# Kernel tuning notes

Hardware: AMD Instinct MI355X
Metric: run time of the kernel (lower is better)

## Reference

```python
import jax, jax.numpy as jnp
import numpy as np

N = 100_000       # total nodes
E = 1_600_000     # edges (avg degree 16)
IN, H, L = 16, 64, 32
G = 100           # graphs
NPG = N // G      # nodes per graph (equal-sized graphs)


def _glorot(key, fan_in, fan_out):
    s = np.sqrt(6.0 / (fan_in + fan_out)).astype(np.float32)
    return jax.random.uniform(key, (fan_in, fan_out), jnp.float32, -s, s)


def setup_inputs() -> dict:
    key = jax.random.key(0)
    ks = jax.random.split(key, 6)
    x = jax.random.normal(ks[0], (N, IN), jnp.float32)
    edge_index = jax.random.randint(ks[1], (2, E), 0, N, dtype=jnp.int64)
    batch = jnp.repeat(jnp.arange(G, dtype=jnp.int64), NPG)  # sorted graph ids
    kw = jax.random.split(ks[2], 4)
    return dict(
        x=x, edge_index=edge_index, batch=batch, nodes_per_graph=NPG,
        W1=_glorot(kw[0], IN, H), b1=jnp.zeros((H,), jnp.float32),
        W2=_glorot(kw[1], H, L), b2=jnp.zeros((L,), jnp.float32),
        W3=_glorot(kw[2], L, H), b3=jnp.zeros((H,), jnp.float32),
        W4=_glorot(kw[3], H, IN), b4=jnp.zeros((IN,), jnp.float32),
    )


def _gcn(x, W, b, src, dst, norm, n):
    # GCNConv: out[dst] += norm_e * (x @ W)[src], plus bias
    h = x @ W
    msg = h[src] * norm[:, None]
    return jax.ops.segment_sum(msg, dst, num_segments=n) + b


def reference(x, edge_index, batch, nodes_per_graph,
              W1, b1, W2, b2, W3, b3, W4, b4):
    n = x.shape[0]
    loops = jnp.arange(n, dtype=edge_index.dtype)
    src = jnp.concatenate([edge_index[0], loops])  # add self-loops (PyG default)
    dst = jnp.concatenate([edge_index[1], loops])
    deg = jax.ops.segment_sum(jnp.ones_like(dst, jnp.float32), dst, num_segments=n)
    dis = jax.lax.rsqrt(jnp.maximum(deg, 1.0))  # deg >= 1 from self-loops
    norm = dis[src] * dis[dst]                   # symmetric normalization

    # encode
    h = jax.nn.relu(_gcn(x, W1, b1, src, dst, norm, n))
    h = _gcn(h, W2, b2, src, dst, norm, n)
    g = n // nodes_per_graph
    sums = jax.ops.segment_sum(h, batch, num_segments=g)
    cnts = jax.ops.segment_sum(jnp.ones((n, 1), jnp.float32), batch, num_segments=g)
    z = sums / cnts                              # global_mean_pool -> [G, L]

    # decode: repeat_interleave(bincount(batch)) with equal graph sizes
    zr = jnp.repeat(z, nodes_per_graph, axis=0)  # [N, L]
    d = jax.nn.relu(_gcn(zr, W3, b3, src, dst, norm, n))
    return _gcn(d, W4, b4, src, dst, norm, n)    # [N, IN]
```

## Files before the change

### kernel.cpp

```cpp
#include <hip/hip_runtime.h>
#include <hip/hip_bf16.h>


constexpr int BSZ_LOG = 9;
constexpr int BSZ     = 1 << BSZ_LOG;
constexpr int NBMAX   = 256;
constexpr int ECHUNK  = 8192;
constexpr int BCAP    = 12288;
constexpr int ZSPLIT  = 8;

__device__ __forceinline__ int gdiv(int v, int npg, float inv) {
    int g = __float2int_rz((float)v * inv);
    int r = v - g * npg;
    if (r < 0) --g; else if (r >= npg) ++g;
    return g;
}

__global__ __launch_bounds__(256)
void binfill_kernel(const int* __restrict__ src, const int* __restrict__ dst,
                    int* __restrict__ bcnt, int* __restrict__ binned, int E) {
    __shared__ int hist[NBMAX], hexcl[NBMAX], gbase[NBMAX], hpos[NBMAX], tmp[NBMAX];
    __shared__ int sorted[ECHUNK];
    __shared__ unsigned char bsorted[ECHUNK];
    int t = threadIdx.x;
    hist[t] = 0; hpos[t] = 0;
    __syncthreads();
    int e0 = blockIdx.x * ECHUNK;
    int cnt = min(ECHUNK, E - e0);
    for (int i = t; i < cnt; i += 256)
        atomicAdd(&hist[dst[e0 + i] >> BSZ_LOG], 1);
    __syncthreads();
    tmp[t] = hist[t];
    __syncthreads();
    for (int d = 1; d < 256; d <<= 1) {
        int v = (t >= d) ? tmp[t - d] : 0;
        __syncthreads();
        tmp[t] += v;
        __syncthreads();
    }
    hexcl[t] = (t == 0) ? 0 : tmp[t - 1];
    int h = hist[t];
    gbase[t] = (h > 0) ? atomicAdd(&bcnt[t], h) : 0;
    __syncthreads();
    for (int i = t; i < cnt; i += 256) {
        int s = src[e0 + i], d = dst[e0 + i];
        int b = d >> BSZ_LOG;
        int code = ((d & (BSZ - 1)) << 20) | s;
        int sp = hexcl[b] + atomicAdd(&hpos[b], 1);
        sorted[sp] = code;
        bsorted[sp] = (unsigned char)b;
    }
    __syncthreads();
    for (int i = t; i < cnt; i += 256) {
        int b = bsorted[i];
        binned[(size_t)b * BCAP + gbase[b] + (i - hexcl[b])] = sorted[i];
    }
}

__device__ __forceinline__ int prefix_before(const int* __restrict__ bcnt,
                                             int b, int* sums) {
    int t = threadIdx.x;
    sums[t] = (t < b) ? bcnt[t] : 0;
    __syncthreads();
    for (int d = 128; d > 0; d >>= 1) {
        if (t < d) sums[t] += sums[t + d];
        __syncthreads();
    }
    int r = sums[0];
    __syncthreads();
    return r;
}

__global__ __launch_bounds__(256)
void csr_off_kernel(const int* __restrict__ binned, const int* __restrict__ bcnt,
                    int* __restrict__ off, float* __restrict__ dis, int n, int E) {
    __shared__ int hist[BSZ];
    __shared__ int lstart[BSZ];
    __shared__ int partial[256];
    int b = blockIdx.x, t = threadIdx.x;
    int nb0 = b << BSZ_LOG;
    int nn = min(BSZ, n - nb0);
    int m = bcnt[b];
    int bs = prefix_before(bcnt, b, partial);
    const int* bp = binned + (size_t)b * BCAP;
    for (int i = t; i < BSZ; i += 256) hist[i] = 0;
    __syncthreads();
    for (int i = t; i < m; i += 256)
        atomicAdd(&hist[bp[i] >> 20], 1);
    __syncthreads();
    int a0 = hist[2 * t], a1 = hist[2 * t + 1];
    partial[t] = a0 + a1;
    __syncthreads();
    for (int d = 1; d < 256; d <<= 1) {
        int v = (t >= d) ? partial[t - d] : 0;
        __syncthreads();
        partial[t] += v;
        __syncthreads();
    }
    int base = (t == 0) ? 0 : partial[t - 1];
    lstart[2 * t] = base;
    lstart[2 * t + 1] = base + a0;
    __syncthreads();
    for (int i = t; i < nn; i += 256) {
        off[nb0 + i] = bs + lstart[i];
        dis[nb0 + i] = rsqrtf((float)hist[i] + 1.0f);
    }
    if (b == 0 && t == 0) off[n] = E;
}

__global__ __launch_bounds__(256)
void bucket_scatter_kernel(const int* __restrict__ binned, const int* __restrict__ bcnt,
                           const float* __restrict__ dis,
                           const int* __restrict__ npg_p, int2* __restrict__ ew, int n) {
    __shared__ int lstart[BSZ];
    __shared__ int lpos[BSZ];
    __shared__ float ldis[BSZ];
    __shared__ int partial[256];
    int b = blockIdx.x, t = threadIdx.x;
    int nb0 = b << BSZ_LOG;
    int nn = min(BSZ, n - nb0);
    int m = bcnt[b];
    int e0 = prefix_before(bcnt, b, partial);
    int npg = npg_p[0];
    float inv = 1.0f / (float)npg;
    const int* bp = binned + (size_t)b * BCAP;
    for (int i = t; i < BSZ; i += 256) {
        lstart[i] = 0; lpos[i] = 0;
        ldis[i] = (i < nn) ? dis[nb0 + i] : 0.f;
    }
    __syncthreads();
    for (int i = t; i < m; i += 256)
        atomicAdd(&lstart[bp[i] >> 20], 1);
    __syncthreads();
    int a0 = lstart[2 * t], a1 = lstart[2 * t + 1];
    partial[t] = a0 + a1;
    __syncthreads();
    for (int d = 1; d < 256; d <<= 1) {
        int v = (t >= d) ? partial[t - d] : 0;
        __syncthreads();
        partial[t] += v;
        __syncthreads();
    }
    int base = (t == 0) ? 0 : partial[t - 1];
    lstart[2 * t] = base;
    lstart[2 * t + 1] = base + a0;
    __syncthreads();
    for (int i = t; i < m; i += 256) {
        int code = bp[i];
        int dl = code >> 20, s = code & 0xFFFFF;
        float w = dis[s] * ldis[dl];
        int g = gdiv(s, npg, inv);
        int p = e0 + lstart[dl] + atomicAdd(&lpos[dl], 1);
        ew[p] = make_int2(s | (g << 20), __float_as_int(w));
    }
}

template <int TPN, bool USE_G>
__device__ __forceinline__ float4
edge_loop(const float4* __restrict__ hp, const int2* __restrict__ ew,
          int e0, int e1, int q, float4 acc) {
    int deg = e1 - e0;
    int nfull = deg / TPN;
    int r = deg - nfull * TPN;
    int idx = e0 + q;
    int2 a = make_int2(0, 0);
    if (idx < e1) a = ew[idx];
    for (int c = 0; c < nfull; ++c) {
        int nidx = idx + (c + 1) * TPN;
        int2 an = make_int2(0, 0);
        if (nidx < e1) an = ew[nidx];
#pragma unroll
        for (int k = 0; k < TPN; ++k) {
            int ax = __shfl(a.x, k, TPN);
            float w = __int_as_float(__shfl(a.y, k, TPN));
            int row = USE_G ? (int)(((unsigned)ax) >> 20) : (ax & 0xFFFFF);
            float4 v = hp[(size_t)row * TPN + q];
            acc.x += w * v.x; acc.y += w * v.y; acc.z += w * v.z; acc.w += w * v.w;
        }
        a = an;
    }
    for (int k = 0; k < r; ++k) {
        int ax = __shfl(a.x, k, TPN);
        float w = __int_as_float(__shfl(a.y, k, TPN));
        int row = USE_G ? (int)(((unsigned)ax) >> 20) : (ax & 0xFFFFF);
        float4 v = hp[(size_t)row * TPN + q];
        acc.x += w * v.x; acc.y += w * v.y; acc.z += w * v.z; acc.w += w * v.w;
    }
    return acc;
}

__global__ __launch_bounds__(256)
void l1w2_kernel(const float* __restrict__ x, const float* __restrict__ dis,
                 const int* __restrict__ off, const int2* __restrict__ ew,
                 const float* __restrict__ W1, const float* __restrict__ b1,
                 const float* __restrict__ W2, float* __restrict__ t2, int n) {
    __shared__ float accs[64][17];
    __shared__ float hl[64][65];
    __shared__ float Wl[16 * 64];
    __shared__ float bl[64];
    int t = threadIdx.x;
    for (int i = t; i < 16 * 64; i += 256) Wl[i] = W1[i];
    if (t < 64) bl[t] = b1[t];

    int q = t & 3, ln = t >> 2;
    int node = blockIdx.x * 64 + ln;
    const float4* xp = (const float4*)x;
    float4 acc = make_float4(0.f, 0.f, 0.f, 0.f);
    if (node < n) {
        float di = dis[node], d2 = di * di;
        float4 v = xp[(size_t)node * 4 + q];
        acc.x = d2 * v.x; acc.y = d2 * v.y; acc.z = d2 * v.z; acc.w = d2 * v.w;
        acc = edge_loop<4, false>(xp, ew, off[node], off[node + 1], q, acc);
    }
    accs[ln][q * 4 + 0] = acc.x; accs[ln][q * 4 + 1] = acc.y;
    accs[ln][q * 4 + 2] = acc.z; accs[ln][q * 4 + 3] = acc.w;
    __syncthreads();

    int j = t & 63;
    for (int nb = (t >> 6); nb < 64; nb += 4) {
        float s = bl[j];
#pragma unroll
        for (int k = 0; k < 16; ++k) s += accs[nb][k] * Wl[k * 64 + j];
        hl[nb][j] = fmaxf(s, 0.f);
    }
    __syncthreads();

    int base = blockIdx.x * 64;
    int c = t & 31;
    for (int nb = (t >> 5); nb < 64; nb += 8) {
        int nd = base + nb;
        if (nd >= n) break;
        float s = 0.f;
#pragma unroll
        for (int k = 0; k < 64; ++k) s += hl[nb][k] * W2[k * 32 + c];
        t2[(size_t)nd * 32 + c] = s;
    }
}

template <int WD>
__global__ __launch_bounds__(256)
void agg_kernel(const float* __restrict__ h, const float* __restrict__ dis,
                const int* __restrict__ off, const int2* __restrict__ ew,
                const float* __restrict__ b, float* __restrict__ out, int n) {
    constexpr int TPN = WD / 4;
    constexpr int NPB = 256 / TPN;
    int t = threadIdx.x;
    int q = t % TPN, ln = t / TPN;
    int node = blockIdx.x * NPB + ln;
    if (node >= n) return;
    const float4* hp = (const float4*)h;
    float di = dis[node], d2 = di * di;
    float4 v = hp[(size_t)node * TPN + q];
    float4 acc;
    acc.x = d2 * v.x; acc.y = d2 * v.y; acc.z = d2 * v.z; acc.w = d2 * v.w;
    acc = edge_loop<TPN, false>(hp, ew, off[node], off[node + 1], q, acc);
    float4 bb = ((const float4*)b)[q];
    float4 o;
    o.x = acc.x + bb.x; o.y = acc.y + bb.y; o.z = acc.z + bb.z; o.w = acc.w + bb.w;
    ((float4*)out)[(size_t)node * TPN + q] = o;
}

__global__ __launch_bounds__(256)
void zagg_kernel(const float* __restrict__ t2, const float* __restrict__ dis,
                 const int* __restrict__ off, const int2* __restrict__ ew,
                 const int* __restrict__ npg_p, float* __restrict__ zsum, int n) {
    __shared__ float4 red0[256];
    __shared__ float4 red1[256];
    int blk = blockIdx.x;
    int b = blk / ZSPLIT, s = blk % ZSPLIT;
    int t = threadIdx.x, q = t & 7, r = t >> 3;
    int npg = npg_p[0];
    int nb0 = b << BSZ_LOG;
    int nn = min(BSZ, n - nb0);
    int g0 = nb0 / npg;
    int nodeB = min((g0 + 1) * npg - nb0, nn);
    int e0 = off[nb0], e1 = off[nb0 + nn];
    int P  = off[nb0 + nodeB];
    int m = e1 - e0;
    const float4* hp = (const float4*)t2;

    float4 a0 = make_float4(0.f, 0.f, 0.f, 0.f);
    float4 a1 = make_float4(0.f, 0.f, 0.f, 0.f);
    int i0 = (int)((long long)m * s / ZSPLIT);
    int i1 = (int)((long long)m * (s + 1) / ZSPLIT);
    for (int i = i0 + r; i < i1; i += 32) {
        int e = e0 + i;
        int2 aa = ew[e];
        float w = __int_as_float(aa.y);
        int src = aa.x & 0xFFFFF;
        float4 v = hp[(size_t)src * 8 + q];
        if (e < P) {
            a0.x += w * v.x; a0.y += w * v.y; a0.z += w * v.z; a0.w += w * v.w;
        } else {
            a1.x += w * v.x; a1.y += w * v.y; a1.z += w * v.z; a1.w += w * v.w;
        }
    }
    int j0 = nn * s / ZSPLIT, j1 = nn * (s + 1) / ZSPLIT;
    for (int i = j0 + r; i < j1; i += 32) {
        int node = nb0 + i;
        float di = dis[node], d2 = di * di;
        float4 v = hp[(size_t)node * 8 + q];
        if (i < nodeB) {
            a0.x += d2 * v.x; a0.y += d2 * v.y; a0.z += d2 * v.z; a0.w += d2 * v.w;
        } else {
            a1.x += d2 * v.x; a1.y += d2 * v.y; a1.z += d2 * v.z; a1.w += d2 * v.w;
        }
    }
    red0[t] = a0; red1[t] = a1;
    __syncthreads();
    for (int d = 128; d >= 8; d >>= 1) {
        if (t < d) {
            float4 u = red0[t], v = red0[t + d];
            u.x += v.x; u.y += v.y; u.z += v.z; u.w += v.w;
            red0[t] = u;
            u = red1[t]; v = red1[t + d];
            u.x += v.x; u.y += v.y; u.z += v.z; u.w += v.w;
            red1[t] = u;
        }
        __syncthreads();
    }
    if (t < 8) {
        float4 v = red0[t];
        atomicAdd(&zsum[g0 * 32 + t * 4 + 0], v.x);
        atomicAdd(&zsum[g0 * 32 + t * 4 + 1], v.y);
        atomicAdd(&zsum[g0 * 32 + t * 4 + 2], v.z);
        atomicAdd(&zsum[g0 * 32 + t * 4 + 3], v.w);
    } else if (t < 16 && nodeB < nn) {
        float4 v = red1[t - 8];
        atomicAdd(&zsum[(g0 + 1) * 32 + (t - 8) * 4 + 0], v.x);
        atomicAdd(&zsum[(g0 + 1) * 32 + (t - 8) * 4 + 1], v.y);
        atomicAdd(&zsum[(g0 + 1) * 32 + (t - 8) * 4 + 2], v.z);
        atomicAdd(&zsum[(g0 + 1) * 32 + (t - 8) * 4 + 3], v.w);
    }
}

__global__ __launch_bounds__(256)
void zred_kernel(const float* __restrict__ zsum, const float* __restrict__ b2,
                 const int* __restrict__ npg_p, float* __restrict__ Z, int n) {
    int npg = npg_p[0];
    int G = n / npg;
    float inv = 1.0f / (float)npg;
    for (int i = blockIdx.x * 256 + threadIdx.x; i < G * 32; i += gridDim.x * 256)
        Z[i] = zsum[i] * inv + b2[i & 31];
}

__global__ __launch_bounds__(256)
void dec1v4_kernel(const float* __restrict__ Z, const float* __restrict__ dis,
                   const int* __restrict__ off, const int2* __restrict__ ew,
                   const int* __restrict__ npg_p, const float* __restrict__ W3,
                   const float* __restrict__ b3, const float* __restrict__ W4,
                   float* __restrict__ t4, int n) {
    __shared__ float zacc[32 * 36];
    __shared__ float hl[32 * 68];
    int t = threadIdx.x;
    int npg = npg_p[0];
    float inv = 1.0f / (float)npg;
    int q = t & 7, ln = t >> 3;
    int base = blockIdx.x * 32;
    int node = base + ln;
    const float4* zp = (const float4*)Z;

    float4 acc = make_float4(0.f, 0.f, 0.f, 0.f);
    if (node < n) {
        float di = dis[node], d2 = di * di;
        int gi = gdiv(node, npg, inv);
        float4 v = zp[(size_t)gi * 8 + q];
        acc.x = d2 * v.x; acc.y = d2 * v.y; acc.z = d2 * v.z; acc.w = d2 * v.w;
        acc = edge_loop<8, true>(zp, ew, off[node], off[node + 1], q, acc);
    }
    zacc[ln * 36 + q * 4 + 0] = acc.x;
    zacc[ln * 36 + q * 4 + 1] = acc.y;
    zacc[ln * 36 + q * 4 + 2] = acc.z;
    zacc[ln * 36 + q * 4 + 3] = acc.w;
    __syncthreads();

    {
        int j = t & 63;
        int i0 = (t >> 6) * 8;
        float w3c[32];
#pragma unroll
        for (int k = 0; k < 32; ++k) w3c[k] = W3[k * 64 + j];
        float bj = b3[j];
        const float4* za4 = (const float4*)zacc;
#pragma unroll
        for (int ii = 0; ii < 8; ++ii) {
            int i = i0 + ii;
            float s = bj;
#pragma unroll
            for (int m = 0; m < 8; ++m) {
                float4 zv = za4[i * 9 + m];
                s += zv.x * w3c[4 * m] + zv.y * w3c[4 * m + 1]
                   + zv.z * w3c[4 * m + 2] + zv.w * w3c[4 * m + 3];
            }
            hl[i * 68 + j] = fmaxf(s, 0.f);
        }
    }
    __syncthreads();

    {
        int c = t & 15;
        int i0 = t >> 4;
        int i1 = i0 + 16;
        const float4* hl4 = (const float4*)hl;
        float s0 = 0.f, s1 = 0.f;
#pragma unroll
        for (int kh = 0; kh < 2; ++kh) {
            float w4c[32];
#pragma unroll
            for (int k = 0; k < 32; ++k) w4c[k] = W4[(kh * 32 + k) * 16 + c];
#pragma unroll
            for (int m = 0; m < 8; ++m) {
                float4 h0 = hl4[i0 * 17 + kh * 8 + m];
                float4 h1 = hl4[i1 * 17 + kh * 8 + m];
                s0 += h0.x * w4c[4 * m] + h0.y * w4c[4 * m + 1]
                    + h0.z * w4c[4 * m + 2] + h0.w * w4c[4 * m + 3];
                s1 += h1.x * w4c[4 * m] + h1.y * w4c[4 * m + 1]
                    + h1.z * w4c[4 * m + 2] + h1.w * w4c[4 * m + 3];
            }
        }
        int nd0 = base + i0, nd1 = base + i1;
        if (nd0 < n) t4[(size_t)nd0 * 16 + c] = s0;
        if (nd1 < n) t4[(size_t)nd1 * 16 + c] = s1;
    }
}

extern "C" void kernel_launch(void* const* d_in, const int* in_sizes, int n_in,
                              void* d_out, int out_size, void* d_ws, size_t ws_size,
                              hipStream_t stream) {
    const float* x     = (const float*)d_in[0];
    const int*   ei    = (const int*)d_in[1];
    const int*   npg   = (const int*)d_in[3];
    const float* W1 = (const float*)d_in[4];
    const float* b1 = (const float*)d_in[5];
    const float* W2 = (const float*)d_in[6];
    const float* b2 = (const float*)d_in[7];
    const float* W3 = (const float*)d_in[8];
    const float* b3 = (const float*)d_in[9];
    const float* W4 = (const float*)d_in[10];
    const float* b4 = (const float*)d_in[11];
    float* out = (float*)d_out;

    int n = in_sizes[0] / 16;
    int E = in_sizes[1] / 2;
    const int* srcp = ei;
    const int* dstp = ei + E;

    char* w = (char*)d_ws;
    auto alloc = [&](size_t bytes) {
        char* p = w;
        w += (bytes + 255) & ~(size_t)255;
        return p;
    };
    float* dis    = (float*)alloc((size_t)n * 4);
    int*   off    = (int*)alloc(((size_t)n + 1) * 4);
    int*   binned = (int*)alloc((size_t)NBMAX * BCAP * 4);
    int2*  ew     = (int2*)alloc((size_t)E * 8);
    float* B      = (float*)alloc((size_t)n * 32 * 4);
    float* Z      = (float*)alloc((size_t)4096 * 32 * 4);
    float* zsum   = (float*)alloc((size_t)4096 * 32 * 4);
    int*   bcnt   = (int*)alloc((size_t)NBMAX * 4);

    int nbuck = (n + BSZ - 1) / BSZ;
    int nbin  = (E + ECHUNK - 1) / ECHUNK;

    hipMemsetAsync(bcnt, 0, (size_t)NBMAX * 4, stream);
    hipMemsetAsync(zsum, 0, (size_t)4096 * 32 * 4, stream);
    binfill_kernel<<<nbin, 256, 0, stream>>>(srcp, dstp, bcnt, binned, E);
    csr_off_kernel<<<nbuck, 256, 0, stream>>>(binned, bcnt, off, dis, n, E);
    bucket_scatter_kernel<<<nbuck, 256, 0, stream>>>(binned, bcnt, dis, npg, ew, n);

    l1w2_kernel<<<(n + 63) / 64, 256, 0, stream>>>(x, dis, off, ew, W1, b1, W2, B, n);
    zagg_kernel<<<nbuck * ZSPLIT, 256, 0, stream>>>(B, dis, off, ew, npg, zsum, n);
    zred_kernel<<<16, 256, 0, stream>>>(zsum, b2, npg, Z, n);

    dec1v4_kernel<<<(n + 31) / 32, 256, 0, stream>>>(Z, dis, off, ew, npg, W3, b3, W4, B, n);
    agg_kernel<16><<<(n + 63) / 64, 256, 0, stream>>>(B, dis, off, ew, b4, out, n);
}
```

Baseline: 218.9 us.

## Store gathered node features in fp16 to halve gather bandwidth

Converts x to fp16 in a new pre-pass and stores the intermediate per-node tensors (layer-2 pre-aggregation and decoder output) as fp16 instead of fp32. All edge gathers in l1w2, zagg and the final aggregation read half-precision rows and accumulate in fp32. This halves the bytes moved by the random gathers over 1.7M edges. It adds a conversion kernel and loses precision in the intermediates.

Measured after the change: 208.7 us. 1.05x faster.

```diff
diff --git a/kernel.cpp b/kernel.cpp
--- a/kernel.cpp
+++ b/kernel.cpp
@@ -1,5 +1,6 @@
 #include <hip/hip_runtime.h>
 #include <hip/hip_bf16.h>
+#include <hip/hip_fp16.h>
 
 
 constexpr int BSZ_LOG = 9;
@@ -8,6 +9,13 @@
 constexpr int ECHUNK  = 8192;
 constexpr int BCAP    = 12288;
 constexpr int ZSPLIT  = 8;
+
+struct alignas(8) h4 { __half2 a, b; };
+
+__device__ __forceinline__ float4 h4_to_f4(h4 v) {
+    float2 fa = __half22float2(v.a), fb = __half22float2(v.b);
+    return make_float4(fa.x, fa.y, fb.x, fb.y);
+}
 
 __device__ __forceinline__ int gdiv(int v, int npg, float inv) {
     int g = __float2int_rz((float)v * inv);
@@ -155,6 +163,52 @@
     }
 }
 
+__global__ __launch_bounds__(256)
+void xconv_kernel(const float* __restrict__ x, h4* __restrict__ xh, int n4) {
+    const float4* xp = (const float4*)x;
+    for (int i = blockIdx.x * 256 + threadIdx.x; i < n4; i += gridDim.x * 256) {
+        float4 v = xp[i];
+        h4 o;
+        o.a = __floats2half2_rn(v.x, v.y);
+        o.b = __floats2half2_rn(v.z, v.w);
+        xh[i] = o;
+    }
+}
+
+template <int TPN, bool USE_G>
+__device__ __forceinline__ float4
+edge_loop_h(const h4* __restrict__ hp, const int2* __restrict__ ew,
+            int e0, int e1, int q, float4 acc) {
+    int deg = e1 - e0;
+    int nfull = deg / TPN;
+    int r = deg - nfull * TPN;
+    int idx = e0 + q;
+    int2 a = make_int2(0, 0);
+    if (idx < e1) a = ew[idx];
+    for (int c = 0; c < nfull; ++c) {
+        int nidx = idx + (c + 1) * TPN;
+        int2 an = make_int2(0, 0);
+        if (nidx < e1) an = ew[nidx];
+#pragma unroll
+        for (int k = 0; k < TPN; ++k) {
+            int ax = __shfl(a.x, k, TPN);
+            float w = __int_as_float(__shfl(a.y, k, TPN));
+            int row = USE_G ? (int)(((unsigned)ax) >> 20) : (ax & 0xFFFFF);
+            float4 v = h4_to_f4(hp[(size_t)row * TPN + q]);
+            acc.x += w * v.x; acc.y += w * v.y; acc.z += w * v.z; acc.w += w * v.w;
+        }
+        a = an;
+    }
+    for (int k = 0; k < r; ++k) {
+        int ax = __shfl(a.x, k, TPN);
+        float w = __int_as_float(__shfl(a.y, k, TPN));
+        int row = USE_G ? (int)(((unsigned)ax) >> 20) : (ax & 0xFFFFF);
+        float4 v = h4_to_f4(hp[(size_t)row * TPN + q]);
+        acc.x += w * v.x; acc.y += w * v.y; acc.z += w * v.z; acc.w += w * v.w;
+    }
+    return acc;
+}
+
 template <int TPN, bool USE_G>
 __device__ __forceinline__ float4
 edge_loop(const float4* __restrict__ hp, const int2* __restrict__ ew,
@@ -190,10 +244,10 @@
 }
 
 __global__ __launch_bounds__(256)
-void l1w2_kernel(const float* __restrict__ x, const float* __restrict__ dis,
+void l1w2_kernel(const h4* __restrict__ xh, const float* __restrict__ dis,
                  const int* __restrict__ off, const int2* __restrict__ ew,
                  const float* __restrict__ W1, const float* __restrict__ b1,
-                 const float* __restrict__ W2, float* __restrict__ t2, int n) {
+                 const float* __restrict__ W2, __half* __restrict__ t2h, int n) {
     __shared__ float accs[64][17];
     __shared__ float hl[64][65];
     __shared__ float Wl[16 * 64];
@@ -204,13 +258,12 @@
 
     int q = t & 3, ln = t >> 2;
     int node = blockIdx.x * 64 + ln;
-    const float4* xp = (const float4*)x;
     float4 acc = make_float4(0.f, 0.f, 0.f, 0.f);
     if (node < n) {
         float di = dis[node], d2 = di * di;
-        float4 v = xp[(size_t)node * 4 + q];
+        float4 v = h4_to_f4(xh[(size_t)node * 4 + q]);
         acc.x = d2 * v.x; acc.y = d2 * v.y; acc.z = d2 * v.z; acc.w = d2 * v.w;
-        acc = edge_loop<4, false>(xp, ew, off[node], off[node + 1], q, acc);
+        acc = edge_loop_h<4, false>(xh, ew, off[node], off[node + 1], q, acc);
     }
     accs[ln][q * 4 + 0] = acc.x; accs[ln][q * 4 + 1] = acc.y;
     accs[ln][q * 4 + 2] = acc.z; accs[ln][q * 4 + 3] = acc.w;
@@ -233,35 +286,31 @@
         float s = 0.f;
 #pragma unroll
         for (int k = 0; k < 64; ++k) s += hl[nb][k] * W2[k * 32 + c];
-        t2[(size_t)nd * 32 + c] = s;
-    }
-}
-
-template <int WD>
-__global__ __launch_bounds__(256)
-void agg_kernel(const float* __restrict__ h, const float* __restrict__ dis,
-                const int* __restrict__ off, const int2* __restrict__ ew,
-                const float* __restrict__ b, float* __restrict__ out, int n) {
-    constexpr int TPN = WD / 4;
-    constexpr int NPB = 256 / TPN;
+        t2h[(size_t)nd * 32 + c] = __float2half(s);
+    }
+}
+
+__global__ __launch_bounds__(256)
+void agg16h_kernel(const h4* __restrict__ t4h, const float* __restrict__ dis,
+                   const int* __restrict__ off, const int2* __restrict__ ew,
+                   const float* __restrict__ b, float* __restrict__ out, int n) {
     int t = threadIdx.x;
-    int q = t % TPN, ln = t / TPN;
-    int node = blockIdx.x * NPB + ln;
+    int q = t & 3, ln = t >> 2;
+    int node = blockIdx.x * 64 + ln;
     if (node >= n) return;
-    const float4* hp = (const float4*)h;
     float di = dis[node], d2 = di * di;
-    float4 v = hp[(size_t)node * TPN + q];
+    float4 v = h4_to_f4(t4h[(size_t)node * 4 + q]);
     float4 acc;
     acc.x = d2 * v.x; acc.y = d2 * v.y; acc.z = d2 * v.z; acc.w = d2 * v.w;
-    acc = edge_loop<TPN, false>(hp, ew, off[node], off[node + 1], q, acc);
+    acc = edge_loop_h<4, false>(t4h, ew, off[node], off[node + 1], q, acc);
     float4 bb = ((const float4*)b)[q];
     float4 o;
     o.x = acc.x + bb.x; o.y = acc.y + bb.y; o.z = acc.z + bb.z; o.w = acc.w + bb.w;
-    ((float4*)out)[(size_t)node * TPN + q] = o;
-}
-
-__global__ __launch_bounds__(256)
-void zagg_kernel(const float* __restrict__ t2, const float* __restrict__ dis,
+    ((float4*)out)[(size_t)node * 4 + q] = o;
+}
+
+__global__ __launch_bounds__(256)
+void zagg_kernel(const h4* __restrict__ t2h, const float* __restrict__ dis,
                  const int* __restrict__ off, const int2* __restrict__ ew,
                  const int* __restrict__ npg_p, float* __restrict__ zsum, int n) {
     __shared__ float4 red0[256];
@@ -277,7 +326,6 @@
     int e0 = off[nb0], e1 = off[nb0 + nn];
     int P  = off[nb0 + nodeB];
     int m = e1 - e0;
-    const float4* hp = (const float4*)t2;
 
     float4 a0 = make_float4(0.f, 0.f, 0.f, 0.f);
     float4 a1 = make_float4(0.f, 0.f, 0.f, 0.f);
@@ -288,7 +336,7 @@
         int2 aa = ew[e];
         float w = __int_as_float(aa.y);
         int src = aa.x & 0xFFFFF;
-        float4 v = hp[(size_t)src * 8 + q];
+        float4 v = h4_to_f4(t2h[(size_t)src * 8 + q]);
         if (e < P) {
             a0.x += w * v.x; a0.y += w * v.y; a0.z += w * v.z; a0.w += w * v.w;
         } else {
@@ -299,7 +347,7 @@
     for (int i = j0 + r; i < j1; i += 32) {
         int node = nb0 + i;
         float di = dis[node], d2 = di * di;
-        float4 v = hp[(size_t)node * 8 + q];
+        float4 v = h4_to_f4(t2h[(size_t)node * 8 + q]);
         if (i < nodeB) {
             a0.x += d2 * v.x; a0.y += d2 * v.y; a0.z += d2 * v.z; a0.w += d2 * v.w;
         } else {
@@ -349,7 +397,7 @@
                    const int* __restrict__ off, const int2* __restrict__ ew,
                    const int* __restrict__ npg_p, const float* __restrict__ W3,
                    const float* __restrict__ b3, const float* __restrict__ W4,
-                   float* __restrict__ t4, int n) {
+                   __half* __restrict__ t4h, int n) {
     __shared__ float zacc[32 * 36];
     __shared__ float hl[32 * 68];
     int t = threadIdx.x;
@@ -419,8 +467,8 @@
             }
         }
         int nd0 = base + i0, nd1 = base + i1;
-        if (nd0 < n) t4[(size_t)nd0 * 16 + c] = s0;
-        if (nd1 < n) t4[(size_t)nd1 * 16 + c] = s1;
+        if (nd0 < n) t4h[(size_t)nd0 * 16 + c] = __float2half(s0);
+        if (nd1 < n) t4h[(size_t)nd1 * 16 + c] = __float2half(s1);
     }
 }
 
@@ -451,28 +499,31 @@
         w += (bytes + 255) & ~(size_t)255;
         return p;
     };
-    float* dis    = (float*)alloc((size_t)n * 4);
-    int*   off    = (int*)alloc(((size_t)n + 1) * 4);
-    int*   binned = (int*)alloc((size_t)NBMAX * BCAP * 4);
-    int2*  ew     = (int2*)alloc((size_t)E * 8);
-    float* B      = (float*)alloc((size_t)n * 32 * 4);
-    float* Z      = (float*)alloc((size_t)4096 * 32 * 4);
-    float* zsum   = (float*)alloc((size_t)4096 * 32 * 4);
-    int*   bcnt   = (int*)alloc((size_t)NBMAX * 4);
+    float*  dis    = (float*)alloc((size_t)n * 4);
+    int*    off    = (int*)alloc(((size_t)n + 1) * 4);
+    int*    binned = (int*)alloc((size_t)NBMAX * BCAP * 4);
+    int2*   ew     = (int2*)alloc((size_t)E * 8);
+    h4*     xh     = (h4*)alloc((size_t)n * 16 * 2);
+    __half* t2h    = (__half*)alloc((size_t)n * 32 * 2);
+    __half* t4h    = (__half*)alloc((size_t)n * 16 * 2);
+    float*  Z      = (float*)alloc((size_t)4096 * 32 * 4);
+    float*  zsum   = (float*)alloc((size_t)4096 * 32 * 4);
+    int*    bcnt   = (int*)alloc((size_t)NBMAX * 4);
 
     int nbuck = (n + BSZ - 1) / BSZ;
     int nbin  = (E + ECHUNK - 1) / ECHUNK;
 
     hipMemsetAsync(bcnt, 0, (size_t)NBMAX * 4, stream);
     hipMemsetAsync(zsum, 0, (size_t)4096 * 32 * 4, stream);
+    xconv_kernel<<<512, 256, 0, stream>>>(x, xh, n * 4);
     binfill_kernel<<<nbin, 256, 0, stream>>>(srcp, dstp, bcnt, binned, E);
     csr_off_kernel<<<nbuck, 256, 0, stream>>>(binned, bcnt, off, dis, n, E);
     bucket_scatter_kernel<<<nbuck, 256, 0, stream>>>(binned, bcnt, dis, npg, ew, n);
 
-    l1w2_kernel<<<(n + 63) / 64, 256, 0, stream>>>(x, dis, off, ew, W1, b1, W2, B, n);
-    zagg_kernel<<<nbuck * ZSPLIT, 256, 0, stream>>>(B, dis, off, ew, npg, zsum, n);
+    l1w2_kernel<<<(n + 63) / 64, 256, 0, stream>>>(xh, dis, off, ew, W1, b1, W2, t2h, n);
+    zagg_kernel<<<nbuck * ZSPLIT, 256, 0, stream>>>((const h4*)t2h, dis, off, ew, npg, zsum, n);
     zred_kernel<<<16, 256, 0, stream>>>(zsum, b2, npg, Z, n);
 
-    dec1v4_kernel<<<(n + 31) / 32, 256, 0, stream>>>(Z, dis, off, ew, npg, W3, b3, W4, B, n);
-    agg_kernel<16><<<(n + 63) / 64, 256, 0, stream>>>(B, dis, off, ew, b4, out, n);
-}
+    dec1v4_kernel<<<(n + 31) / 32, 256, 0, stream>>>(Z, dis, off, ew, npg, W3, b3, W4, t4h, n);
+    agg16h_kernel<<<(n + 63) / 64, 256, 0, stream>>>((const h4*)t4h, dis, off, ew, b4, out, n);
+}
```
